# Optimization experiments

Hardware: AMD Instinct MI355X
Metric: run time of the kernel (lower is better)

The kernel has to match this reference:

```python
import jax, jax.numpy as jnp
import numpy as np

H = 8      # n_heads
E = 128    # d_keys (== D; required by out_projection Linear(D*n_heads, D))


def setup_inputs() -> dict:
    key = jax.random.key(0)
    ks = jax.random.split(key, 11)
    B, T, D = 64, 256, 128
    s = 0.02
    return {
        "x": jax.random.normal(ks[0], (B, T, D), dtype=jnp.float32),
        "Wq": jax.random.normal(ks[1], (D, H * E), dtype=jnp.float32) * s,
        "bq": jax.random.normal(ks[2], (H * E,), dtype=jnp.float32) * s,
        "Wk": jax.random.normal(ks[3], (D, H * E), dtype=jnp.float32) * s,
        "bk": jax.random.normal(ks[4], (H * E,), dtype=jnp.float32) * s,
        "Wv": jax.random.normal(ks[5], (D, H * E), dtype=jnp.float32) * s,
        "bv": jax.random.normal(ks[6], (H * E,), dtype=jnp.float32) * s,
        "Ws": jax.random.normal(ks[7], (T, 1), dtype=jnp.float32) * s,
        "bs": jax.random.normal(ks[8], (1,), dtype=jnp.float32) * s,
        "Wo": jax.random.normal(ks[9], (H * E, D), dtype=jnp.float32) * s,
        "bo": jax.random.normal(ks[10], (D,), dtype=jnp.float32) * s,
    }


def reference(x, Wq, bq, Wk, bk, Wv, bv, Ws, bs, Wo, bo):
    B, T, D = x.shape
    # Q/K/V projections -> [B, T, H, E]
    Q = (x @ Wq + bq).reshape(B, T, H, E)
    K = (x @ Wk + bk).reshape(B, T, H, E)
    V = (x @ Wv + bv).reshape(B, T, H, E)
    scale = 1.0 / jnp.sqrt(jnp.float32(E))
    # QK^T scores over time: [B, H, T, T] (query t, key j)
    scores = jnp.einsum('bthd,bjhd->bhtj', Q, K)
    # summary projection contracts the key axis j: T -> 1  => [B, H, T, 1]
    summary = (scale * scores) @ Ws + bs
    # softmax over the query axis t (dim=-2)
    beta = jax.nn.softmax(summary, axis=-2)[..., 0]        # [B, H, T]
    # weight V per (b, t, h) and sum over time -> [B, H, E]
    beta_cal = jnp.transpose(beta, (0, 2, 1))[..., None]   # [B, T, H, 1]
    result = jnp.sum(V * beta_cal, axis=1)                 # [B, H, E]
    out = result.reshape(B, H * E) @ Wo + bo               # [B, D]
    return out
```

## Files before the change

### kernel.cpp

```cpp
#include <hip/hip_runtime.h>
#include <hip/hip_bf16.h>


#define SCALE 0.08838834764831845f
#define MAGIC 0x13579BDFu

__global__ __launch_bounds__(512)
void ta_one(const float* __restrict__ x,  const float* __restrict__ Wq,
            const float* __restrict__ Wk, const float* __restrict__ bk,
            const float* __restrict__ Wv, const float* __restrict__ bv,
            const float* __restrict__ Wsv,
            const float* __restrict__ Wo, const float* __restrict__ bov,
            float* __restrict__ ws, float* __restrict__ out)
{
    __shared__ __align__(16) float Tf[9216];
    __shared__ __align__(16) float red[2][256];
    __shared__ __align__(16) float wsS[256];
    __shared__ __align__(16) float xwS[128];
    __shared__ __align__(16) float kwS[256];
    __shared__ __align__(16) float wqkS[256];
    __shared__ __align__(16) float betaS[2][256];
    __shared__ __align__(16) float xbS[256];
    __shared__ __align__(16) float resS[256];
    __shared__ float smx[2][4], sms[2][4];
    __shared__ float swS;

    const int tid = threadIdx.x;
    const int b = blockIdx.x, p = blockIdx.y;
    const int w = tid >> 6, l = tid & 63;
    const float* xp0 = x + (size_t)b * 32768;

    if (tid < 256) wsS[tid] = Wsv[tid];
    __syncthreads();

    {
        const int q = tid & 31, tc = tid >> 5;
        float4 acc = {0.f, 0.f, 0.f, 0.f};
        const float4* xp = (const float4*)(xp0 + (size_t)(tc * 16) * 128 + 4 * q);
        #pragma unroll
        for (int j = 0; j < 16; ++j) {
            const float4 xv = xp[(size_t)j * 32];
            const float wsv = wsS[tc * 16 + j];
            acc.x += wsv * xv.x; acc.y += wsv * xv.y;
            acc.z += wsv * xv.z; acc.w += wsv * xv.w;
        }
        *(float4*)(Tf + tc * 128 + 4 * q) = acc;
        __syncthreads();
        if (tid < 128) {
            float v = 0.f;
            #pragma unroll
            for (int g = 0; g < 16; ++g) v += Tf[g * 128 + tid];
            xwS[tid] = v;
        } else if (tid < 192) {
            float v = wsS[l] + wsS[l + 64] + wsS[l + 128] + wsS[l + 192];
            #pragma unroll
            for (int off = 32; off; off >>= 1) v += __shfl_xor(v, off, 64);
            if (l == 0) swS = v;
        }
        __syncthreads();
    }

    {
        const int q = tid & 63, kh = tid >> 6;
        float4 acc = {0.f, 0.f, 0.f, 0.f};
        const float4* wp = (const float4*)(Wk + (size_t)(kh * 16) * 1024 + 256 * p + 4 * q);
        #pragma unroll
        for (int j = 0; j < 16; ++j) {
            const float4 wv = wp[(size_t)j * 256];
            const float xv = xwS[kh * 16 + j];
            acc.x += xv * wv.x; acc.y += xv * wv.y;
            acc.z += xv * wv.z; acc.w += xv * wv.w;
        }
        *(float4*)(Tf + kh * 256 + 4 * q) = acc;
        __syncthreads();
        if (tid < 256) {
            float v = swS * bk[256 * p + tid];
            #pragma unroll
            for (int g = 0; g < 8; ++g) v += Tf[g * 256 + tid];
            kwS[tid] = v;
        }
        __syncthreads();
    }

    {
        const int o = tid & 255, eh = tid >> 8;
        float acc = 0.f;
        for (int tau = 0; tau < 4; ++tau) {
            __syncthreads();
            #pragma unroll
            for (int r = 0; r < 4; ++r) {
                const int f4 = tid + 512 * r;
                const int oo = f4 >> 3, j4 = f4 & 7;
                const float4 v = *(const float4*)(Wq + (size_t)(oo & 127) * 1024
                                    + (2 * p + (oo >> 7)) * 128 + tau * 32 + 4 * j4);
                *(float4*)(Tf + oo * 36 + 4 * j4) = v;
            }
            __syncthreads();
            #pragma unroll
            for (int j4 = eh * 4; j4 < eh * 4 + 4; ++j4) {
                const float4 t4 = *(const float4*)(Tf + o * 36 + 4 * j4);
                const float4 k4 = *(const float4*)(kwS + (o >> 7) * 128 + tau * 32 + 4 * j4);
                acc += t4.x * k4.x + t4.y * k4.y + t4.z * k4.z + t4.w * k4.w;
            }
        }
        red[eh][o] = acc;
        __syncthreads();
        if (tid < 256) wqkS[tid] = (red[0][tid] + red[1][tid]) * SCALE;
        __syncthreads();
    }

    {
        const int t = tid & 255, hi = tid >> 8;
        float acc = 0.f;
        for (int tau = 0; tau < 4; ++tau) {
            __syncthreads();
            #pragma unroll
            for (int r = 0; r < 4; ++r) {
                const int f4 = tid + 512 * r;
                const int tt = f4 >> 3, j4 = f4 & 7;
                const float4 v = *(const float4*)(xp0 + (size_t)tt * 128 + tau * 32 + 4 * j4);
                *(float4*)(Tf + tt * 36 + 4 * j4) = v;
            }
            __syncthreads();
            #pragma unroll
            for (int j4 = 0; j4 < 8; ++j4) {
                const float4 t4 = *(const float4*)(Tf + t * 36 + 4 * j4);
                const float4 q4 = *(const float4*)(wqkS + hi * 128 + tau * 32 + 4 * j4);
                acc += t4.x * q4.x + t4.y * q4.y + t4.z * q4.z + t4.w * q4.w;
            }
        }
        betaS[hi][t] = acc;
        __syncthreads();
    }

    {
        const int t = tid & 255, hi = tid >> 8;
        const float v = betaS[hi][t];
        float m = v;
        #pragma unroll
        for (int off = 32; off; off >>= 1) m = fmaxf(m, __shfl_xor(m, off, 64));
        if (l == 0) smx[hi][w & 3] = m;
        __syncthreads();
        const float M = fmaxf(fmaxf(smx[hi][0], smx[hi][1]), fmaxf(smx[hi][2], smx[hi][3]));
        const float e = __expf(v - M);
        float ssum = e;
        #pragma unroll
        for (int off = 32; off; off >>= 1) ssum += __shfl_xor(ssum, off, 64);
        if (l == 0) sms[hi][w & 3] = ssum;
        __syncthreads();
        const float S = sms[hi][0] + sms[hi][1] + sms[hi][2] + sms[hi][3];
        betaS[hi][t] = e / S;
        __syncthreads();
    }

    {
        const int q = tid & 31, tc = tid >> 5;
        float4 a0 = {0.f,0.f,0.f,0.f}, a1 = {0.f,0.f,0.f,0.f};
        const float4* xp = (const float4*)(xp0 + (size_t)(tc * 16) * 128 + 4 * q);
        #pragma unroll
        for (int j = 0; j < 16; ++j) {
            const float4 xv = xp[(size_t)j * 32];
            const float b0 = betaS[0][tc * 16 + j], b1 = betaS[1][tc * 16 + j];
            a0.x += b0 * xv.x; a0.y += b0 * xv.y; a0.z += b0 * xv.z; a0.w += b0 * xv.w;
            a1.x += b1 * xv.x; a1.y += b1 * xv.y; a1.z += b1 * xv.z; a1.w += b1 * xv.w;
        }
        *(float4*)(Tf + tc * 128 + 4 * q) = a0;
        *(float4*)(Tf + 2048 + tc * 128 + 4 * q) = a1;
        __syncthreads();
        if (tid < 256) {
            const int hi = tid >> 7, d = tid & 127;
            float v = 0.f;
            #pragma unroll
            for (int g = 0; g < 16; ++g) v += Tf[hi * 2048 + g * 128 + d];
            xbS[tid] = v;
        }
        __syncthreads();
    }

    {
        const int q = tid & 63, kh = tid >> 6;
        const int hi = q >> 5;
        float4 acc = {0.f, 0.f, 0.f, 0.f};
        const float4* wp = (const float4*)(Wv + (size_t)(kh * 16) * 1024 + 256 * p + 4 * q);
        #pragma unroll
        for (int j = 0; j < 16; ++j) {
            const float4 wv = wp[(size_t)j * 256];
            const float xv = xbS[hi * 128 + kh * 16 + j];
            acc.x += xv * wv.x; acc.y += xv * wv.y;
            acc.z += xv * wv.z; acc.w += xv * wv.w;
        }
        __syncthreads();
        *(float4*)(Tf + kh * 256 + 4 * q) = acc;
        __syncthreads();
        if (tid < 256) {
            float v = bv[256 * p + tid];
            #pragma unroll
            for (int g = 0; g < 8; ++g) v += Tf[g * 256 + tid];
            resS[tid] = v;
        }
        __syncthreads();
    }

    {
        const int q = tid & 31, rh = tid >> 5;
        float4 acc = {0.f, 0.f, 0.f, 0.f};
        const float4* wp = (const float4*)(Wo + (size_t)(256 * p + rh * 16) * 128 + 4 * q);
        #pragma unroll
        for (int j = 0; j < 16; ++j) {
            const float4 wv = wp[(size_t)j * 32];
            const float rv = resS[rh * 16 + j];
            acc.x += rv * wv.x; acc.y += rv * wv.y;
            acc.z += rv * wv.z; acc.w += rv * wv.w;
        }
        *(float4*)(Tf + rh * 128 + 4 * q) = acc;
        __syncthreads();
    }

    float* part = ws;
    unsigned* flags = (unsigned*)(ws + 32768);
    if (p < 3) {
        if (tid < 128) {
            float v = 0.f;
            #pragma unroll
            for (int g = 0; g < 16; ++g) v += Tf[g * 128 + tid];
            part[(size_t)(b * 4 + p) * 128 + tid] = v;
            __threadfence();
        }
        __syncthreads();
        if (tid == 0) atomicExch(&flags[b * 4 + p], MAGIC);
    } else {
        if (tid == 0) {
            while (atomicCAS(&flags[b * 4 + 0], MAGIC, MAGIC) != MAGIC) {}
            while (atomicCAS(&flags[b * 4 + 1], MAGIC, MAGIC) != MAGIC) {}
            while (atomicCAS(&flags[b * 4 + 2], MAGIC, MAGIC) != MAGIC) {}
        }
        __syncthreads();
        if (tid < 128) {
            float v = bov[tid];
            #pragma unroll
            for (int g = 0; g < 16; ++g) v += Tf[g * 128 + tid];
            v += atomicAdd(&part[(size_t)(b * 4 + 0) * 128 + tid], 0.f);
            v += atomicAdd(&part[(size_t)(b * 4 + 1) * 128 + tid], 0.f);
            v += atomicAdd(&part[(size_t)(b * 4 + 2) * 128 + tid], 0.f);
            out[(size_t)b * 128 + tid] = v;
        }
    }
}

extern "C" void kernel_launch(void* const* d_in, const int* in_sizes, int n_in,
                              void* d_out, int out_size, void* d_ws, size_t ws_size,
                              hipStream_t stream) {
    const float* x  = (const float*)d_in[0];
    const float* Wq = (const float*)d_in[1];
    const float* Wk = (const float*)d_in[3];
    const float* bk = (const float*)d_in[4];
    const float* Wv = (const float*)d_in[5];
    const float* bv = (const float*)d_in[6];
    const float* Ws = (const float*)d_in[7];
    const float* Wo = (const float*)d_in[9];
    const float* bo = (const float*)d_in[10];
    float* out = (float*)d_out;
    float* ws  = (float*)d_ws;

    ta_one<<<dim3(64, 4), dim3(512), 0, stream>>>(x, Wq, Wk, bk, Wv, bv, Ws, Wo, bo, ws, out);
}
```

Measured before the change: 99.34 us.

## Prefetch global operands into registers ahead of each stage to overlap loads

```diff
diff --git a/kernel.cpp b/kernel.cpp
--- a/kernel.cpp
+++ b/kernel.cpp
@@ -13,8 +13,8 @@
             const float* __restrict__ Wo, const float* __restrict__ bov,
             float* __restrict__ ws, float* __restrict__ out)
 {
-    __shared__ __align__(16) float Tf[9216];
-    __shared__ __align__(16) float red[2][256];
+    __shared__ __align__(16) float pA[2056];
+    __shared__ __align__(16) float pB[2056];
     __shared__ __align__(16) float wsS[256];
     __shared__ __align__(16) float xwS[128];
     __shared__ __align__(16) float kwS[256];
@@ -30,112 +30,153 @@
     const int w = tid >> 6, l = tid & 63;
     const float* xp0 = x + (size_t)b * 32768;
 
-    if (tid < 256) wsS[tid] = Wsv[tid];
-    __syncthreads();
-
-    {
-        const int q = tid & 31, tc = tid >> 5;
+    const int q5 = tid & 31, tc = tid >> 5;
+    const int q6 = tid & 63, kh = tid >> 6;
+    const int c8 = tid & 7,  r8 = tid >> 3;
+
+    float4 rx[16];
+    {
+        const float4* xp = (const float4*)(xp0 + (size_t)(tc * 16) * 128 + 4 * q5);
+        #pragma unroll
+        for (int j = 0; j < 16; ++j) rx[j] = xp[(size_t)j * 32];
+    }
+    float4 rwk[16];
+    {
+        const float4* wp = (const float4*)(Wk + (size_t)(kh * 16) * 1024 + 256 * p + 4 * q6);
+        #pragma unroll
+        for (int j = 0; j < 16; ++j) rwk[j] = wp[(size_t)j * 256];
+    }
+    const float bkv = bk[256 * p + (tid & 255)];
+    const float bvv = bv[256 * p + (tid & 255)];
+    if (tid < 64) *(float4*)(wsS + 4 * tid) = *(const float4*)(Wsv + 4 * tid);
+    __syncthreads();
+
+    {
         float4 acc = {0.f, 0.f, 0.f, 0.f};
-        const float4* xp = (const float4*)(xp0 + (size_t)(tc * 16) * 128 + 4 * q);
-        #pragma unroll
-        for (int j = 0; j < 16; ++j) {
-            const float4 xv = xp[(size_t)j * 32];
-            const float wsv = wsS[tc * 16 + j];
-            acc.x += wsv * xv.x; acc.y += wsv * xv.y;
-            acc.z += wsv * xv.z; acc.w += wsv * xv.w;
-        }
-        *(float4*)(Tf + tc * 128 + 4 * q) = acc;
-        __syncthreads();
-        if (tid < 128) {
-            float v = 0.f;
-            #pragma unroll
-            for (int g = 0; g < 16; ++g) v += Tf[g * 128 + tid];
-            xwS[tid] = v;
-        } else if (tid < 192) {
-            float v = wsS[l] + wsS[l + 64] + wsS[l + 128] + wsS[l + 192];
-            #pragma unroll
-            for (int off = 32; off; off >>= 1) v += __shfl_xor(v, off, 64);
-            if (l == 0) swS = v;
-        }
-        __syncthreads();
-    }
-
-    {
-        const int q = tid & 63, kh = tid >> 6;
+        #pragma unroll
+        for (int j = 0; j < 16; ++j) {
+            const float s = wsS[tc * 16 + j];
+            acc.x += s * rx[j].x; acc.y += s * rx[j].y;
+            acc.z += s * rx[j].z; acc.w += s * rx[j].w;
+        }
+        *(float4*)(pA + tc * 128 + 4 * q5) = acc;
+    }
+    float4 rwq[16];
+    {
+        #pragma unroll
+        for (int rr = 0; rr < 4; ++rr) {
+            const int o = r8 + 64 * rr;
+            const float* base = Wq + (size_t)(o & 127) * 1024 + (2 * p + (o >> 7)) * 128;
+            #pragma unroll
+            for (int jj = 0; jj < 4; ++jj)
+                rwq[rr * 4 + jj] = *(const float4*)(base + (jj * 8 + c8) * 4);
+        }
+    }
+    __syncthreads();
+    if (tid < 128) {
+        float v = 0.f;
+        #pragma unroll
+        for (int g = 0; g < 16; ++g) v += pA[g * 128 + tid];
+        xwS[tid] = v;
+    } else if (tid < 192) {
+        float v = wsS[l] + wsS[l + 64] + wsS[l + 128] + wsS[l + 192];
+        #pragma unroll
+        for (int off = 32; off; off >>= 1) v += __shfl_xor(v, off, 64);
+        if (l == 0) swS = v;
+    }
+    __syncthreads();
+
+    {
         float4 acc = {0.f, 0.f, 0.f, 0.f};
-        const float4* wp = (const float4*)(Wk + (size_t)(kh * 16) * 1024 + 256 * p + 4 * q);
-        #pragma unroll
-        for (int j = 0; j < 16; ++j) {
-            const float4 wv = wp[(size_t)j * 256];
+        #pragma unroll
+        for (int j = 0; j < 16; ++j) {
             const float xv = xwS[kh * 16 + j];
-            acc.x += xv * wv.x; acc.y += xv * wv.y;
-            acc.z += xv * wv.z; acc.w += xv * wv.w;
-        }
-        *(float4*)(Tf + kh * 256 + 4 * q) = acc;
-        __syncthreads();
-        if (tid < 256) {
-            float v = swS * bk[256 * p + tid];
-            #pragma unroll
-            for (int g = 0; g < 8; ++g) v += Tf[g * 256 + tid];
-            kwS[tid] = v;
-        }
-        __syncthreads();
-    }
-
-    {
-        const int o = tid & 255, eh = tid >> 8;
-        float acc = 0.f;
-        for (int tau = 0; tau < 4; ++tau) {
-            __syncthreads();
-            #pragma unroll
-            for (int r = 0; r < 4; ++r) {
-                const int f4 = tid + 512 * r;
-                const int oo = f4 >> 3, j4 = f4 & 7;
-                const float4 v = *(const float4*)(Wq + (size_t)(oo & 127) * 1024
-                                    + (2 * p + (oo >> 7)) * 128 + tau * 32 + 4 * j4);
-                *(float4*)(Tf + oo * 36 + 4 * j4) = v;
+            acc.x += xv * rwk[j].x; acc.y += xv * rwk[j].y;
+            acc.z += xv * rwk[j].z; acc.w += xv * rwk[j].w;
+        }
+        *(float4*)(pB + kh * 256 + 4 * q6) = acc;
+    }
+    float4 rxd[16];
+    {
+        #pragma unroll
+        for (int rr = 0; rr < 4; ++rr) {
+            const int t = r8 + 64 * rr;
+            const float* base = xp0 + (size_t)t * 128;
+            #pragma unroll
+            for (int jj = 0; jj < 4; ++jj)
+                rxd[rr * 4 + jj] = *(const float4*)(base + (jj * 8 + c8) * 4);
+        }
+    }
+    __syncthreads();
+    if (tid < 256) {
+        float v = swS * bkv;
+        #pragma unroll
+        for (int g = 0; g < 8; ++g) v += pB[g * 256 + tid];
+        kwS[tid] = v;
+    }
+    __syncthreads();
+
+    {
+        #pragma unroll
+        for (int rr = 0; rr < 4; ++rr) {
+            const int o = r8 + 64 * rr;
+            const float* kp = kwS + (o >> 7) * 128;
+            float a = 0.f;
+            #pragma unroll
+            for (int jj = 0; jj < 4; ++jj) {
+                const float4 wv = rwq[rr * 4 + jj];
+                const float* kk = kp + (jj * 8 + c8) * 4;
+                a += wv.x * kk[0] + wv.y * kk[1] + wv.z * kk[2] + wv.w * kk[3];
             }
-            __syncthreads();
-            #pragma unroll
-            for (int j4 = eh * 4; j4 < eh * 4 + 4; ++j4) {
-                const float4 t4 = *(const float4*)(Tf + o * 36 + 4 * j4);
-                const float4 k4 = *(const float4*)(kwS + (o >> 7) * 128 + tau * 32 + 4 * j4);
-                acc += t4.x * k4.x + t4.y * k4.y + t4.z * k4.z + t4.w * k4.w;
+            pA[c8 * 257 + o] = a;
+        }
+    }
+    float4 rwv[16];
+    {
+        const float4* wp = (const float4*)(Wv + (size_t)(kh * 16) * 1024 + 256 * p + 4 * q6);
+        #pragma unroll
+        for (int j = 0; j < 16; ++j) rwv[j] = wp[(size_t)j * 256];
+    }
+    __syncthreads();
+    if (tid < 256) {
+        float v = 0.f;
+        #pragma unroll
+        for (int g = 0; g < 8; ++g) v += pA[g * 257 + tid];
+        wqkS[tid] = v * SCALE;
+    }
+    __syncthreads();
+
+    {
+        #pragma unroll
+        for (int rr = 0; rr < 4; ++rr) {
+            const int t = r8 + 64 * rr;
+            float a0 = 0.f, a1 = 0.f;
+            #pragma unroll
+            for (int jj = 0; jj < 4; ++jj) {
+                const float4 xv = rxd[rr * 4 + jj];
+                const float* q0 = wqkS + (jj * 8 + c8) * 4;
+                const float* q1 = wqkS + 128 + (jj * 8 + c8) * 4;
+                a0 += xv.x * q0[0] + xv.y * q0[1] + xv.z * q0[2] + xv.w * q0[3];
+                a1 += xv.x * q1[0] + xv.y * q1[1] + xv.z * q1[2] + xv.w * q1[3];
             }
-        }
-        red[eh][o] = acc;
-        __syncthreads();
-        if (tid < 256) wqkS[tid] = (red[0][tid] + red[1][tid]) * SCALE;
-        __syncthreads();
-    }
+            pA[c8 * 257 + t] = a0;
+            pB[c8 * 257 + t] = a1;
+        }
+    }
+    float4 rxe[16];
+    {
+        const float4* xp = (const float4*)(xp0 + (size_t)(tc * 16) * 128 + 4 * q5);
+        #pragma unroll
+        for (int j = 0; j < 16; ++j) rxe[j] = xp[(size_t)j * 32];
+    }
+    __syncthreads();
 
     {
         const int t = tid & 255, hi = tid >> 8;
-        float acc = 0.f;
-        for (int tau = 0; tau < 4; ++tau) {
-            __syncthreads();
-            #pragma unroll
-            for (int r = 0; r < 4; ++r) {
-                const int f4 = tid + 512 * r;
-                const int tt = f4 >> 3, j4 = f4 & 7;
-                const float4 v = *(const float4*)(xp0 + (size_t)tt * 128 + tau * 32 + 4 * j4);
-                *(float4*)(Tf + tt * 36 + 4 * j4) = v;
-            }
-            __syncthreads();
-            #pragma unroll
-            for (int j4 = 0; j4 < 8; ++j4) {
-                const float4 t4 = *(const float4*)(Tf + t * 36 + 4 * j4);
-                const float4 q4 = *(const float4*)(wqkS + hi * 128 + tau * 32 + 4 * j4);
-                acc += t4.x * q4.x + t4.y * q4.y + t4.z * q4.z + t4.w * q4.w;
-            }
-        }
-        betaS[hi][t] = acc;
-        __syncthreads();
-    }
-
-    {
-        const int t = tid & 255, hi = tid >> 8;
-        const float v = betaS[hi][t];
+        const float* pS = hi ? pB : pA;
+        float v = 0.f;
+        #pragma unroll
+        for (int g = 0; g < 8; ++g) v += pS[g * 257 + t];
         float m = v;
         #pragma unroll
         for (int off = 32; off; off >>= 1) m = fmaxf(m, __shfl_xor(m, off, 64));
@@ -154,67 +195,66 @@
     }
 
     {
-        const int q = tid & 31, tc = tid >> 5;
         float4 a0 = {0.f,0.f,0.f,0.f}, a1 = {0.f,0.f,0.f,0.f};
-        const float4* xp = (const float4*)(xp0 + (size_t)(tc * 16) * 128 + 4 * q);
-        #pragma unroll
-        for (int j = 0; j < 16; ++j) {
-            const float4 xv = xp[(size_t)j * 32];
+        #pragma unroll
+        for (int j = 0; j < 16; ++j) {
             const float b0 = betaS[0][tc * 16 + j], b1 = betaS[1][tc * 16 + j];
-            a0.x += b0 * xv.x; a0.y += b0 * xv.y; a0.z += b0 * xv.z; a0.w += b0 * xv.w;
-            a1.x += b1 * xv.x; a1.y += b1 * xv.y; a1.z += b1 * xv.z; a1.w += b1 * xv.w;
-        }
-        *(float4*)(Tf + tc * 128 + 4 * q) = a0;
-        *(float4*)(Tf + 2048 + tc * 128 + 4 * q) = a1;
-        __syncthreads();
-        if (tid < 256) {
-            const int hi = tid >> 7, d = tid & 127;
-            float v = 0.f;
-            #pragma unroll
-            for (int g = 0; g < 16; ++g) v += Tf[hi * 2048 + g * 128 + d];
-            xbS[tid] = v;
-        }
-        __syncthreads();
-    }
-
-    {
-        const int q = tid & 63, kh = tid >> 6;
-        const int hi = q >> 5;
+            a0.x += b0 * rxe[j].x; a0.y += b0 * rxe[j].y;
+            a0.z += b0 * rxe[j].z; a0.w += b0 * rxe[j].w;
+            a1.x += b1 * rxe[j].x; a1.y += b1 * rxe[j].y;
+            a1.z += b1 * rxe[j].z; a1.w += b1 * rxe[j].w;
+        }
+        *(float4*)(pA + tc * 128 + 4 * q5) = a0;
+        *(float4*)(pB + tc * 128 + 4 * q5) = a1;
+    }
+    __syncthreads();
+    if (tid < 256) {
+        const int hi = tid >> 7, d = tid & 127;
+        const float* pp = hi ? pB : pA;
+        float v = 0.f;
+        #pragma unroll
+        for (int g = 0; g < 16; ++g) v += pp[g * 128 + d];
+        xbS[tid] = v;
+    }
+    __syncthreads();
+
+    {
+        const int hi = q6 >> 5;
         float4 acc = {0.f, 0.f, 0.f, 0.f};
-        const float4* wp = (const float4*)(Wv + (size_t)(kh * 16) * 1024 + 256 * p + 4 * q);
-        #pragma unroll
-        for (int j = 0; j < 16; ++j) {
-            const float4 wv = wp[(size_t)j * 256];
+        #pragma unroll
+        for (int j = 0; j < 16; ++j) {
             const float xv = xbS[hi * 128 + kh * 16 + j];
-            acc.x += xv * wv.x; acc.y += xv * wv.y;
-            acc.z += xv * wv.z; acc.w += xv * wv.w;
-        }
-        __syncthreads();
-        *(float4*)(Tf + kh * 256 + 4 * q) = acc;
-        __syncthreads();
-        if (tid < 256) {
-            float v = bv[256 * p + tid];
-            #pragma unroll
-            for (int g = 0; g < 8; ++g) v += Tf[g * 256 + tid];
-            resS[tid] = v;
-        }
-        __syncthreads();
-    }
-
-    {
-        const int q = tid & 31, rh = tid >> 5;
+            acc.x += xv * rwv[j].x; acc.y += xv * rwv[j].y;
+            acc.z += xv * rwv[j].z; acc.w += xv * rwv[j].w;
+        }
+        *(float4*)(pB + kh * 256 + 4 * q6) = acc;
+    }
+    float4 rwo[16];
+    {
+        const float4* wp = (const float4*)(Wo + (size_t)(256 * p + tc * 16) * 128 + 4 * q5);
+        #pragma unroll
+        for (int j = 0; j < 16; ++j) rwo[j] = wp[(size_t)j * 32];
+    }
+    __syncthreads();
+    if (tid < 256) {
+        float v = bvv;
+        #pragma unroll
+        for (int g = 0; g < 8; ++g) v += pB[g * 256 + tid];
+        resS[tid] = v;
+    }
+    __syncthreads();
+
+    {
         float4 acc = {0.f, 0.f, 0.f, 0.f};
-        const float4* wp = (const float4*)(Wo + (size_t)(256 * p + rh * 16) * 128 + 4 * q);
-        #pragma unroll
-        for (int j = 0; j < 16; ++j) {
-            const float4 wv = wp[(size_t)j * 32];
-            const float rv = resS[rh * 16 + j];
-            acc.x += rv * wv.x; acc.y += rv * wv.y;
-            acc.z += rv * wv.z; acc.w += rv * wv.w;
-        }
-        *(float4*)(Tf + rh * 128 + 4 * q) = acc;
-        __syncthreads();
-    }
+        #pragma unroll
+        for (int j = 0; j < 16; ++j) {
+            const float rv = resS[tc * 16 + j];
+            acc.x += rv * rwo[j].x; acc.y += rv * rwo[j].y;
+            acc.z += rv * rwo[j].z; acc.w += rv * rwo[j].w;
+        }
+        *(float4*)(pA + tc * 128 + 4 * q5) = acc;
+    }
+    __syncthreads();
 
     float* part = ws;
     unsigned* flags = (unsigned*)(ws + 32768);
@@ -222,7 +262,7 @@
         if (tid < 128) {
             float v = 0.f;
             #pragma unroll
-            for (int g = 0; g < 16; ++g) v += Tf[g * 128 + tid];
+            for (int g = 0; g < 16; ++g) v += pA[g * 128 + tid];
             part[(size_t)(b * 4 + p) * 128 + tid] = v;
             __threadfence();
         }
@@ -238,7 +278,7 @@
         if (tid < 128) {
             float v = bov[tid];
             #pragma unroll
-            for (int g = 0; g < 16; ++g) v += Tf[g * 128 + tid];
+            for (int g = 0; g < 16; ++g) v += pA[g * 128 + tid];
             v += atomicAdd(&part[(size_t)(b * 4 + 0) * 128 + tid], 0.f);
             v += atomicAdd(&part[(size_t)(b * 4 + 1) * 128 + tid], 0.f);
             v += atomicAdd(&part[(size_t)(b * 4 + 2) * 128 + tid], 0.f);
```

Measured after the change: 96.69 us. 1.03x faster.
